# Performance work log

Measured on AMD Instinct MI355X. Metric: run time of the kernel, lower is better.

Reference implementation:

```python
import jax, jax.numpy as jnp
import numpy as np

C = 128
GROUPS = 8
EPS = 1e-5


def setup_inputs() -> dict:
    key = jax.random.key(0)
    ks = jax.random.split(key, 7)
    B, D, H, W = 2, 8, 32, 32
    x = jax.random.normal(ks[0], (B, C, D, H, W), dtype=jnp.float32)
    gamma = jnp.ones((C,), dtype=jnp.float32)
    beta = jnp.zeros((C,), dtype=jnp.float32)
    w_qkv = jax.random.normal(ks[1], (3 * C, C), dtype=jnp.float32) * 0.02
    b_qkv = jnp.zeros((3 * C,), dtype=jnp.float32)
    w_proj = jax.random.normal(ks[2], (C, C), dtype=jnp.float32) * 0.02
    b_proj = jnp.zeros((C,), dtype=jnp.float32)
    return {"x": x, "gamma": gamma, "beta": beta, "w_qkv": w_qkv,
            "b_qkv": b_qkv, "w_proj": w_proj, "b_proj": b_proj}


def _group_norm(x, gamma, beta):
    B, Cc, D, H, W = x.shape
    xg = x.reshape(B, GROUPS, Cc // GROUPS, D, H, W)
    mean = jnp.mean(xg, axis=(2, 3, 4, 5), keepdims=True)
    var = jnp.var(xg, axis=(2, 3, 4, 5), keepdims=True)
    xn = (xg - mean) * jax.lax.rsqrt(var + EPS)
    xn = xn.reshape(B, Cc, D, H, W)
    return xn * gamma[None, :, None, None, None] + beta[None, :, None, None, None]


def reference(x, gamma, beta, w_qkv, b_qkv, w_proj, b_proj):
    B, Cc, D, H, W = x.shape
    N = D * H * W
    h = _group_norm(x, gamma, beta)
    # 1x1x1 conv == per-voxel matmul over channels
    qkv = jnp.einsum('bcdhw,oc->bodhw', h, w_qkv) + b_qkv[None, :, None, None, None]
    q, k, v = jnp.split(qkv, 3, axis=1)  # each [B, C, D, H, W]
    q = q.reshape(B, Cc, N).transpose(0, 2, 1)  # [B, N, C]
    k = k.reshape(B, Cc, N).transpose(0, 2, 1)
    v = v.reshape(B, Cc, N).transpose(0, 2, 1)
    scale = Cc ** (-0.5)
    attn = jax.nn.softmax(jnp.einsum('bnc,bmc->bnm', q, k) * scale, axis=-1)
    h = jnp.einsum('bnm,bmc->bnc', attn, v)  # [B, N, C]
    h = h.transpose(0, 2, 1).reshape(B, Cc, D, H, W)
    out = jnp.einsum('bcdhw,oc->bodhw', h, w_proj) + b_proj[None, :, None, None, None]
    return x + out
```

## Files before the change

### kernel.cpp

```cpp
#include <hip/hip_runtime.h>

typedef __bf16 bf16x8 __attribute__((ext_vector_type(8)));
typedef float  f32x4  __attribute__((ext_vector_type(4)));
typedef float  f32x16 __attribute__((ext_vector_type(16)));
typedef float  f32x2  __attribute__((ext_vector_type(2)));
typedef unsigned int uint32;
typedef unsigned int u32x2 __attribute__((ext_vector_type(2)));
typedef int i32x4 __attribute__((ext_vector_type(4)));
typedef int i32x8 __attribute__((ext_vector_type(8)));
typedef long long i64;
typedef long long i64x4v __attribute__((ext_vector_type(4)));

#define MFMA16(a, b, c) __builtin_amdgcn_mfma_f32_16x16x32_bf16((a), (b), (c), 0, 0, 0)
#define MFMA32F8(a, b, c) __builtin_amdgcn_mfma_f32_32x32x16_fp8_fp8((a), (b), (c), 0, 0, 0)
#define GLL(gsrc, ldst) __builtin_amdgcn_global_load_lds( \
    (const __attribute__((address_space(1))) uint32*)(gsrc), \
    (__attribute__((address_space(3))) uint32*)(ldst), 16, 0, 0)

static constexpr int Cch = 128;
static constexpr int Nvox = 8192;

__device__ inline f32x16 mx4(i32x8 a, i32x8 b, f32x16 c) {
#if __has_builtin(__builtin_amdgcn_mfma_scale_f32_32x32x64_f8f6f4)
  return __builtin_amdgcn_mfma_scale_f32_32x32x64_f8f6f4(
      a, b, c, 0 , 0 ,
      0, 0x7F7F7F7Fu ,
      0, 0x7F7F7F7Fu );
#else
  i64x4v av = __builtin_bit_cast(i64x4v, a);
  i64x4v bv = __builtin_bit_cast(i64x4v, b);
  c = MFMA32F8(av[0], bv[0], c);
  c = MFMA32F8(av[1], bv[1], c);
  c = MFMA32F8(av[2], bv[2], c);
  c = MFMA32F8(av[3], bv[3], c);
  return c;
#endif
}

__device__ inline unsigned int pkbf(float x, float y) {
  unsigned short ux = __builtin_bit_cast(unsigned short, (__bf16)x);
  unsigned short uy = __builtin_bit_cast(unsigned short, (__bf16)y);
  return (unsigned int)ux | ((unsigned int)uy << 16);
}

__device__ inline unsigned int pk4fp8(float a, float b, float c, float d) {
  int w = 0;
  w = __builtin_amdgcn_cvt_pk_fp8_f32(a, b, w, false);
  w = __builtin_amdgcn_cvt_pk_fp8_f32(c, d, w, true);
  return (unsigned int)w;
}
__device__ inline unsigned char fp8b(float x) {
  return (unsigned char)(__builtin_amdgcn_cvt_pk_fp8_f32(x, x, 0, false) & 0xff);
}

__device__ inline void lane32_swap(unsigned int& x, unsigned int& y) {
#if __has_builtin(__builtin_amdgcn_permlane32_swap)
  auto r = __builtin_amdgcn_permlane32_swap(x, y, false, false);
  x = r[0]; y = r[1];
#else
  unsigned int sx = (unsigned int)__shfl_xor((int)x, 32);
  unsigned int sy = (unsigned int)__shfl_xor((int)y, 32);
  bool lo = ((threadIdx.x & 63) < 32);
  unsigned int nx = lo ? x : sy;
  unsigned int ny = lo ? sx : y;
  x = nx; y = ny;
#endif
}
__device__ inline float red32_sum(float v) {
  unsigned int a = __builtin_bit_cast(unsigned int, v), b = a;
  lane32_swap(a, b);
  return __builtin_bit_cast(float, a) + __builtin_bit_cast(float, b);
}

__global__ __launch_bounds__(256) void gn_part_k(const float* __restrict__ x,
                                                 f32x2* __restrict__ part) {
  int bg = blockIdx.x >> 4, pt = blockIdx.x & 15;
  const f32x4* xb = (const f32x4*)(x + (size_t)bg * 131072 + (size_t)pt * 8192);
  float s = 0.f, ss = 0.f;
  for (int i = threadIdx.x; i < 2048; i += 256) {
    f32x4 v = xb[i];
    s += (v.x + v.y) + (v.z + v.w);
    ss += (v.x * v.x + v.y * v.y) + (v.z * v.z + v.w * v.w);
  }
#pragma unroll
  for (int off = 32; off; off >>= 1) {
    s  += __shfl_down(s, off);
    ss += __shfl_down(ss, off);
  }
  __shared__ float rb[4], rbss[4];
  if ((threadIdx.x & 63) == 0) { rb[threadIdx.x >> 6] = s; rbss[threadIdx.x >> 6] = ss; }
  __syncthreads();
  if (threadIdx.x == 0) {
    f32x2 o; o.x = rb[0] + rb[1] + rb[2] + rb[3];
    o.y = rbss[0] + rbss[1] + rbss[2] + rbss[3];
    part[blockIdx.x] = o;
  }
}

__global__ __launch_bounds__(256) void gn_fin_k(const f32x2* __restrict__ part,
                                                float* __restrict__ stats) {
  int tid = threadIdx.x;
  f32x2 v = part[tid];
  float s = v.x, ss = v.y;
#pragma unroll
  for (int off = 1; off < 16; off <<= 1) {
    s += __shfl_xor(s, off);
    ss += __shfl_xor(ss, off);
  }
  if ((tid & 15) == 0) {
    int bg = tid >> 4;
    const float invn = 1.f / 131072.f;
    float mean = s * invn;
    float var = ss * invn - mean * mean;
    stats[bg] = mean;
    stats[16 + bg] = rsqrtf(var + 1e-5f);
  }
}

__global__ __launch_bounds__(256) void conv_w_k(const float* __restrict__ wq,
                                                const float* __restrict__ wp,
                                                __bf16* __restrict__ wqb,
                                                __bf16* __restrict__ wpb) {
  int i = blockIdx.x * 256 + threadIdx.x;
  if (i < 384 * 128) wqb[i] = (__bf16)wq[i];
  if (i < 128 * 128) wpb[i] = (__bf16)wp[i];
}

__global__ __launch_bounds__(256) void gn_apply_k(const float* __restrict__ x,
                                                  const float* __restrict__ gamma,
                                                  const float* __restrict__ beta,
                                                  const float* __restrict__ stats,
                                                  __bf16* __restrict__ xn) {
  __shared__ __bf16 t[64][136];
  int b = blockIdx.x >> 7;
  int n0 = (blockIdx.x & 127) << 6;
  const float* xb = x + (size_t)b * Cch * Nvox;
  for (int i = threadIdx.x; i < 128 * 64; i += 256) {
    int c = i >> 6, nl = i & 63;
    int g = c >> 4;
    float mean = stats[b * 8 + g];
    float rstd = stats[16 + b * 8 + g];
    float v = xb[(size_t)c * Nvox + n0 + nl];
    t[nl][c] = (__bf16)((v - mean) * rstd * gamma[c] + beta[c]);
  }
  __syncthreads();
  __bf16* outb = xn + (size_t)b * Nvox * Cch;
  for (int i = threadIdx.x; i < 64 * 16; i += 256) {
    int row = i >> 4, ch = (i & 15) << 3;
    *reinterpret_cast<bf16x8*>(&outb[(size_t)(n0 + row) * Cch + ch]) =
        *reinterpret_cast<const bf16x8*>(&t[row][ch]);
  }
}

__global__ __launch_bounds__(256) void qkv_k(const __bf16* __restrict__ xn,
                                             const __bf16* __restrict__ wq,
                                             const float* __restrict__ b_qkv,
                                             unsigned char* __restrict__ q8,
                                             unsigned char* __restrict__ k8,
                                             unsigned char* __restrict__ v8t) {
  int id = blockIdx.x;
  int b = id / 768;
  int rr = id % 768;
  int o0b = (rr >> 7) * 64;
  int n0 = (rr & 127) * 64;
  int w = threadIdx.x >> 6, l = threadIdx.x & 63;
  int lr = l & 15, lh = l >> 4;
  int ow = o0b + w * 16;
  const float k2 = 0.08838834764831845f * 1.4426950408889634f;

  bf16x8 a[4];
#pragma unroll
  for (int kc = 0; kc < 4; kc++)
    a[kc] = *reinterpret_cast<const bf16x8*>(&wq[(size_t)(ow + lr) * 128 + kc * 32 + lh * 8]);

  const __bf16* xb = xn + (size_t)b * Nvox * Cch;
#pragma unroll
  for (int ns = 0; ns < 4; ns++) {
    f32x4 acc = {0.f, 0.f, 0.f, 0.f};
#pragma unroll
    for (int kc = 0; kc < 4; kc++) {
      bf16x8 bf = *reinterpret_cast<const bf16x8*>(
          &xb[(size_t)(n0 + ns * 16 + lr) * Cch + kc * 32 + lh * 8]);
      acc = MFMA16(a[kc], bf, acc);
    }
    int o0 = ow + lh * 4;
    int n = n0 + ns * 16 + lr;
    float f0 = acc[0] + b_qkv[o0 + 0];
    float f1 = acc[1] + b_qkv[o0 + 1];
    float f2 = acc[2] + b_qkv[o0 + 2];
    float f3 = acc[3] + b_qkv[o0 + 3];
    if (o0 < 128) {
      *reinterpret_cast<unsigned int*>(
          q8 + ((size_t)b * Nvox + n) * 128 + o0) =
          pk4fp8(f0 * k2, f1 * k2, f2 * k2, f3 * k2);
    } else if (o0 < 256) {
      *reinterpret_cast<unsigned int*>(
          k8 + ((size_t)b * Nvox + n) * 128 + (o0 - 128)) = pk4fp8(f0, f1, f2, f3);
    } else {
      int c0 = o0 - 256;
      int kk = n & 63;
      int r4 = kk & 15;
      int hh = (r4 >> 2) & 1;
      int jj = (r4 & 3) + (((r4 >> 3) & 1) << 2);
      int m = ((kk >> 5) << 5) + (hh << 4) + (((kk >> 4) & 1) << 3) + jj;
      int nst = (n & ~63) | m;
      v8t[((size_t)b * Cch + c0 + 0) * Nvox + nst] = fp8b(f0);
      v8t[((size_t)b * Cch + c0 + 1) * Nvox + nst] = fp8b(f1);
      v8t[((size_t)b * Cch + c0 + 2) * Nvox + nst] = fp8b(f2);
      v8t[((size_t)b * Cch + c0 + 3) * Nvox + nst] = fp8b(f3);
    }
  }
}

__global__ __launch_bounds__(256, 2) void attn_k(const unsigned char* __restrict__ q,
                                                 const unsigned char* __restrict__ kk,
                                                 const unsigned char* __restrict__ vt,
                                                 __bf16* __restrict__ po0,
                                                 __bf16* __restrict__ po1,
                                                 __bf16* __restrict__ po2,
                                                 __bf16* __restrict__ po3,
                                                 f32x2* __restrict__ ml) {
  extern __shared__ char smem[];
  const int bi = blockIdx.x;
  const int kq = bi & 3;
  const int b = (bi >> 2) & 1;
  const int qgrp = bi >> 3;
  const int w = threadIdx.x >> 6;
  const int l = threadIdx.x & 63;
  const int l31 = l & 31, h = l >> 5;
  const int swl16 = (l31 & 15) << 4;

  const char* kbase = (const char*)kk + ((size_t)b * 8192 + (size_t)kq * 2048) * 128;
  const char* vbase = (const char*)vt + (size_t)b * 1048576 + (size_t)kq * 2048;

  const unsigned char* qrow = q +
      ((size_t)b * 8192 + (size_t)qgrp * 128 + (size_t)w * 32 + l31) * 128 + h * 32;
  i32x8 qa8[2];
#pragma unroll
  for (int dc = 0; dc < 2; dc++) {
    i32x4 q0 = *reinterpret_cast<const i32x4*>(qrow + dc * 64);
    i32x4 q1 = *reinterpret_cast<const i32x4*>(qrow + dc * 64 + 16);
    qa8[dc] = __builtin_shufflevector(q0, q1, 0, 1, 2, 3, 4, 5, 6, 7);
  }

  f32x16 O[4];
#pragma unroll
  for (int cb = 0; cb < 4; cb++)
#pragma unroll
    for (int r = 0; r < 16; r++) O[cb][r] = 0.f;
  float s0 = 0.f, s1 = 0.f, s2 = 0.f, s3 = 0.f;

  auto stage = [&](int t, int bs) {
    if (w < 2) {
      const char* kt = kbase + (size_t)t * 64 * 128;
      char* dst = smem + bs * 16384;
#pragma unroll
      for (int it = 0; it < 4; ++it) {
        int ob = (w * 4 + it) * 1024;
        int o = ob + l * 16;
        int row = o >> 8;
        int lcol = (o & 255) ^ ((row & 15) << 4);
        int ksel = lcol >> 7, c = lcol & 127;
        GLL(kt + (size_t)(ksel * 32 + row) * 128 + c, dst + ob);
      }
    } else {
      const char* vtile = vbase + (size_t)t * 64;
      char* dst = smem + bs * 16384 + 8192;
#pragma unroll
      for (int it = 0; it < 4; ++it) {
        int ob = ((w - 2) * 4 + it) * 1024;
        int o = ob + l * 16;
        int row = o >> 8;
        int lcol = (o & 255) ^ ((row & 15) << 4);
        int cs = lcol >> 6, k16 = lcol & 63;
        GLL(vtile + (size_t)(cs * 32 + row) * 8192 + k16, dst + ob);
      }
    }
  };

  stage(0, 0);
  int cur = 0;
  const int NT = 32;

  for (int t = 0; t < NT; ++t) {
    asm volatile("s_waitcnt vmcnt(0) lgkmcnt(0)" ::: "memory");
    __builtin_amdgcn_sched_barrier(0);
    __syncthreads();
    if (t + 1 < NT) stage(t + 1, cur ^ 1);

    const char* Kb = smem + cur * 16384;
    const char* Vb = Kb + 8192;

    f32x16 St[2];
#pragma unroll
    for (int ks = 0; ks < 2; ks++)
#pragma unroll
      for (int r = 0; r < 16; r++) St[ks][r] = 0.f;
    __builtin_amdgcn_s_setprio(1);
#pragma unroll
    for (int ks = 0; ks < 2; ks++) {
#pragma unroll
      for (int dc = 0; dc < 2; dc++) {
        int base = ks * 128 + dc * 64 + h * 32;
        i32x4 k0 = *reinterpret_cast<const i32x4*>(
            Kb + (size_t)l31 * 256 + (base ^ swl16));
        i32x4 k1 = *reinterpret_cast<const i32x4*>(
            Kb + (size_t)l31 * 256 + ((base + 16) ^ swl16));
        St[ks] = mx4(__builtin_shufflevector(k0, k1, 0, 1, 2, 3, 4, 5, 6, 7),
                     qa8[dc], St[ks]);
      }
    }
    __builtin_amdgcn_s_setprio(0);

#pragma unroll
    for (int ks = 0; ks < 2; ks++)
#pragma unroll
      for (int r = 0; r < 16; r++)
        St[ks][r] = __builtin_amdgcn_exp2f(St[ks][r]);
#pragma unroll
    for (int ks = 0; ks < 2; ks++)
#pragma unroll
      for (int r = 0; r < 16; r += 4) {
        s0 += St[ks][r + 0]; s1 += St[ks][r + 1];
        s2 += St[ks][r + 2]; s3 += St[ks][r + 3];
      }

    i32x8 pb;
#pragma unroll
    for (int ks = 0; ks < 2; ks++) {
      pb[ks * 4 + 0] = (int)pk4fp8(St[ks][0],  St[ks][1],  St[ks][2],  St[ks][3]);
      pb[ks * 4 + 1] = (int)pk4fp8(St[ks][4],  St[ks][5],  St[ks][6],  St[ks][7]);
      pb[ks * 4 + 2] = (int)pk4fp8(St[ks][8],  St[ks][9],  St[ks][10], St[ks][11]);
      pb[ks * 4 + 3] = (int)pk4fp8(St[ks][12], St[ks][13], St[ks][14], St[ks][15]);
    }

    __builtin_amdgcn_s_setprio(1);
#pragma unroll
    for (int cb = 0; cb < 4; cb++) {
      int vb0 = cb * 64 + h * 16;
      i32x4 v0 = *reinterpret_cast<const i32x4*>(
          Vb + (size_t)l31 * 256 + (vb0 ^ swl16));
      i32x4 v1 = *reinterpret_cast<const i32x4*>(
          Vb + (size_t)l31 * 256 + ((vb0 + 32) ^ swl16));
      O[cb] = mx4(__builtin_shufflevector(v0, v1, 0, 1, 2, 3, 4, 5, 6, 7),
                  pb, O[cb]);
    }
    __builtin_amdgcn_s_setprio(0);
    cur ^= 1;
  }

  float lsum = red32_sum((s0 + s1) + (s2 + s3));
  __bf16* po = (kq == 0) ? po0 : (kq == 1) ? po1 : (kq == 2) ? po2 : po3;
  int qg = b * 8192 + qgrp * 128 + w * 32 + l31;
#pragma unroll
  for (int cb = 0; cb < 4; cb++) {
#pragma unroll
    for (int rq = 0; rq < 4; rq++) {
      int c = cb * 32 + rq * 8 + h * 4;
      u32x2 wv;
      wv[0] = pkbf(O[cb][rq * 4 + 0], O[cb][rq * 4 + 1]);
      wv[1] = pkbf(O[cb][rq * 4 + 2], O[cb][rq * 4 + 3]);
      *reinterpret_cast<u32x2*>((char*)po + ((size_t)qg * 128 + c) * 2) = wv;
    }
  }
  if (l < 32) {
    f32x2 v; v.x = 0.f; v.y = lsum;
    ml[(size_t)kq * 16384 + qg] = v;
  }
}

__global__ __launch_bounds__(256) void proj_k(const __bf16* __restrict__ po0,
                                              const __bf16* __restrict__ po1,
                                              const __bf16* __restrict__ po2,
                                              const __bf16* __restrict__ po3,
                                              const f32x2* __restrict__ ml,
                                              const __bf16* __restrict__ wp,
                                              const float* __restrict__ b_proj,
                                              const float* __restrict__ x,
                                              float* __restrict__ out) {
  int id = blockIdx.x;
  int b = id >> 8;
  int co0 = ((id >> 7) & 1) * 64;
  int n0 = (id & 127) * 64;
  int w = threadIdx.x >> 6, l = threadIdx.x & 63;
  int lr = l & 15, lh = l >> 4;
  int cow = co0 + w * 16;

  bf16x8 a[4];
#pragma unroll
  for (int kc = 0; kc < 4; kc++)
    a[kc] = *reinterpret_cast<const bf16x8*>(&wp[(size_t)(cow + lr) * 128 + kc * 32 + lh * 8]);

#pragma unroll
  for (int ns = 0; ns < 4; ns++) {
    int n = n0 + ns * 16 + lr;
    int qg = b * 8192 + n;
    f32x2 a0 = ml[qg], a1 = ml[16384 + qg], a2 = ml[32768 + qg], a3 = ml[49152 + qg];
    float M = fmaxf(fmaxf(a0.x, a1.x), fmaxf(a2.x, a3.x));
    float e0 = __builtin_amdgcn_exp2f(a0.x - M);
    float e1 = __builtin_amdgcn_exp2f(a1.x - M);
    float e2 = __builtin_amdgcn_exp2f(a2.x - M);
    float e3 = __builtin_amdgcn_exp2f(a3.x - M);
    float invL = 1.f / (e0 * a0.y + e1 * a1.y + e2 * a2.y + e3 * a3.y);
    float c0f = e0 * invL, c1f = e1 * invL, c2f = e2 * invL, c3f = e3 * invL;

    f32x4 acc = {0.f, 0.f, 0.f, 0.f};
#pragma unroll
    for (int kc = 0; kc < 4; kc++) {
      size_t off = (size_t)qg * 128 + kc * 32 + lh * 8;
      bf16x8 v0 = *reinterpret_cast<const bf16x8*>(&po0[off]);
      bf16x8 v1 = *reinterpret_cast<const bf16x8*>(&po1[off]);
      bf16x8 v2 = *reinterpret_cast<const bf16x8*>(&po2[off]);
      bf16x8 v3 = *reinterpret_cast<const bf16x8*>(&po3[off]);
      bf16x8 hv;
#pragma unroll
      for (int i = 0; i < 8; i++)
        hv[i] = (__bf16)(c0f * (float)v0[i] + c1f * (float)v1[i] +
                         c2f * (float)v2[i] + c3f * (float)v3[i]);
      acc = MFMA16(a[kc], hv, acc);
    }
#pragma unroll
    for (int r2 = 0; r2 < 4; r2++) {
      int co = cow + lh * 4 + r2;
      size_t idx = ((size_t)b * Cch + co) * Nvox + n;
      out[idx] = x[idx] + b_proj[co] + acc[r2];
    }
  }
}

extern "C" void kernel_launch(void* const* d_in, const int* in_sizes, int n_in,
                              void* d_out, int out_size, void* d_ws, size_t ws_size,
                              hipStream_t stream) {
  const float* x      = (const float*)d_in[0];
  const float* gamma  = (const float*)d_in[1];
  const float* beta   = (const float*)d_in[2];
  const float* w_qkv  = (const float*)d_in[3];
  const float* b_qkv  = (const float*)d_in[4];
  const float* w_proj = (const float*)d_in[5];
  const float* b_proj = (const float*)d_in[6];
  float* out = (float*)d_out;

  char* ws = (char*)d_ws;
  float*  stats = (float*)ws;
  f32x2*  part  = (f32x2*)(ws + 256);
  __bf16* wq_b  = (__bf16*)(ws + 4096);
  __bf16* wp_b  = (__bf16*)(ws + 4096 + 98304);
  size_t base = 135168;
  const size_t SZ = (size_t)2 * Nvox * Cch * sizeof(__bf16);
  __bf16* xn  = (__bf16*)(ws + base + 0 * SZ);
  unsigned char* q8  = (unsigned char*)(ws + base + 1 * SZ);
  unsigned char* k8  = (unsigned char*)(ws + base + 2 * SZ);
  unsigned char* v8t = (unsigned char*)(ws + base + 3 * SZ);
  __bf16* hw  = (__bf16*)(ws + base + 4 * SZ);
  f32x2*  ml  = (f32x2*)(ws + base + 5 * SZ);
  __bf16* po2 = (__bf16*)(ws + base + 5 * SZ + 524288);
  __bf16* po3 = (__bf16*)(ws + base + 5 * SZ + 524288 + SZ);

  (void)hipFuncSetAttribute((const void*)attn_k,
                            hipFuncAttributeMaxDynamicSharedMemorySize, 32768);

  gn_part_k<<<256, 256, 0, stream>>>(x, part);
  gn_fin_k<<<1, 256, 0, stream>>>(part, stats);
  conv_w_k<<<192, 256, 0, stream>>>(w_qkv, w_proj, wq_b, wp_b);
  gn_apply_k<<<256, 256, 0, stream>>>(x, gamma, beta, stats, xn);
  qkv_k<<<1536, 256, 0, stream>>>(xn, wq_b, b_qkv, q8, k8, v8t);
  attn_k<<<512, 256, 32768, stream>>>(q8, k8, v8t, hw, xn, po2, po3, ml);
  proj_k<<<512, 256, 0, stream>>>(hw, xn, po2, po3, ml, wp_b, b_proj, x, out);
}
```

Before: 96.83 us.

## Split attention KV into eight chunks, store fp8 partials, fuse small prep kernels

Attention now splits keys into 8 chunks of 1024 instead of 4 of 2048, launches 1024 blocks with a launch bound of 4 blocks per unit, and writes partial outputs as fp8 plus a single row-sum float. The max term was already fixed at zero, so the proj kernel just sums the partials and divides by the total L. The weight conversion kernel is folded into gn_part_k, and the group-norm finalize kernel is folded into gn_apply_k, removing two launches. The goal is better occupancy and less partial-output traffic, at the cost of fp8 rounding on the partial outputs and redundant stats work in every apply block.

```diff
diff --git a/kernel.cpp b/kernel.cpp
--- a/kernel.cpp
+++ b/kernel.cpp
@@ -24,8 +24,7 @@
 #if __has_builtin(__builtin_amdgcn_mfma_scale_f32_32x32x64_f8f6f4)
   return __builtin_amdgcn_mfma_scale_f32_32x32x64_f8f6f4(
       a, b, c, 0 , 0 ,
-      0, 0x7F7F7F7Fu ,
-      0, 0x7F7F7F7Fu );
+      0, 0x7F7F7F7Fu, 0, 0x7F7F7F7Fu );
 #else
   i64x4v av = __builtin_bit_cast(i64x4v, a);
   i64x4v bv = __builtin_bit_cast(i64x4v, b);
@@ -37,12 +36,6 @@
 #endif
 }
 
-__device__ inline unsigned int pkbf(float x, float y) {
-  unsigned short ux = __builtin_bit_cast(unsigned short, (__bf16)x);
-  unsigned short uy = __builtin_bit_cast(unsigned short, (__bf16)y);
-  return (unsigned int)ux | ((unsigned int)uy << 16);
-}
-
 __device__ inline unsigned int pk4fp8(float a, float b, float c, float d) {
   int w = 0;
   w = __builtin_amdgcn_cvt_pk_fp8_f32(a, b, w, false);
@@ -51,6 +44,22 @@
 }
 __device__ inline unsigned char fp8b(float x) {
   return (unsigned char)(__builtin_amdgcn_cvt_pk_fp8_f32(x, x, 0, false) & 0xff);
+}
+template <bool HI>
+__device__ inline f32x2 dec2fp8(unsigned int w) {
+#if __has_builtin(__builtin_amdgcn_cvt_pk_f32_fp8)
+  return __builtin_amdgcn_cvt_pk_f32_fp8((int)w, HI);
+#else
+  f32x2 r;
+#pragma unroll
+  for (int j = 0; j < 2; j++) {
+    unsigned char v = (unsigned char)(w >> ((HI ? 2 : 0) + j) * 8);
+    unsigned int e = (v >> 3) & 15, m = v & 7;
+    float mag = e ? ldexpf((float)(8 + m), (int)e - 10) : ldexpf((float)m, -9);
+    r[j] = (v & 0x80) ? -mag : mag;
+  }
+  return r;
+#endif
 }
 
 __device__ inline void lane32_swap(unsigned int& x, unsigned int& y) {
@@ -73,7 +82,15 @@
 }
 
 __global__ __launch_bounds__(256) void gn_part_k(const float* __restrict__ x,
-                                                 f32x2* __restrict__ part) {
+                                                 f32x2* __restrict__ part,
+                                                 const float* __restrict__ wq,
+                                                 const float* __restrict__ wp,
+                                                 __bf16* __restrict__ wqb,
+                                                 __bf16* __restrict__ wpb) {
+  int wi = blockIdx.x * 256 + threadIdx.x;
+  if (wi < 49152) wqb[wi] = (__bf16)wq[wi];
+  else wpb[wi - 49152] = (__bf16)wp[wi - 49152];
+
   int bg = blockIdx.x >> 4, pt = blockIdx.x & 15;
   const f32x4* xb = (const f32x4*)(x + (size_t)bg * 131072 + (size_t)pt * 8192);
   float s = 0.f, ss = 0.f;
@@ -97,49 +114,40 @@
   }
 }
 
-__global__ __launch_bounds__(256) void gn_fin_k(const f32x2* __restrict__ part,
-                                                float* __restrict__ stats) {
-  int tid = threadIdx.x;
-  f32x2 v = part[tid];
-  float s = v.x, ss = v.y;
-#pragma unroll
-  for (int off = 1; off < 16; off <<= 1) {
-    s += __shfl_xor(s, off);
-    ss += __shfl_xor(ss, off);
-  }
-  if ((tid & 15) == 0) {
-    int bg = tid >> 4;
-    const float invn = 1.f / 131072.f;
-    float mean = s * invn;
-    float var = ss * invn - mean * mean;
-    stats[bg] = mean;
-    stats[16 + bg] = rsqrtf(var + 1e-5f);
-  }
-}
-
-__global__ __launch_bounds__(256) void conv_w_k(const float* __restrict__ wq,
-                                                const float* __restrict__ wp,
-                                                __bf16* __restrict__ wqb,
-                                                __bf16* __restrict__ wpb) {
-  int i = blockIdx.x * 256 + threadIdx.x;
-  if (i < 384 * 128) wqb[i] = (__bf16)wq[i];
-  if (i < 128 * 128) wpb[i] = (__bf16)wp[i];
-}
-
 __global__ __launch_bounds__(256) void gn_apply_k(const float* __restrict__ x,
                                                   const float* __restrict__ gamma,
                                                   const float* __restrict__ beta,
-                                                  const float* __restrict__ stats,
+                                                  const f32x2* __restrict__ part,
                                                   __bf16* __restrict__ xn) {
   __shared__ __bf16 t[64][136];
+  __shared__ float sm_mean[16], sm_rstd[16];
+  int tid = threadIdx.x;
+  {
+    f32x2 v = part[tid];
+    float s = v.x, ss = v.y;
+#pragma unroll
+    for (int off = 1; off < 16; off <<= 1) {
+      s += __shfl_xor(s, off);
+      ss += __shfl_xor(ss, off);
+    }
+    if ((tid & 15) == 0) {
+      int bg = tid >> 4;
+      const float invn = 1.f / 131072.f;
+      float mean = s * invn;
+      float var = ss * invn - mean * mean;
+      sm_mean[bg] = mean;
+      sm_rstd[bg] = rsqrtf(var + 1e-5f);
+    }
+  }
+  __syncthreads();
   int b = blockIdx.x >> 7;
   int n0 = (blockIdx.x & 127) << 6;
   const float* xb = x + (size_t)b * Cch * Nvox;
   for (int i = threadIdx.x; i < 128 * 64; i += 256) {
     int c = i >> 6, nl = i & 63;
     int g = c >> 4;
-    float mean = stats[b * 8 + g];
-    float rstd = stats[16 + b * 8 + g];
+    float mean = sm_mean[b * 8 + g];
+    float rstd = sm_rstd[b * 8 + g];
     float v = xb[(size_t)c * Nvox + n0 + nl];
     t[nl][c] = (__bf16)((v - mean) * rstd * gamma[c] + beta[c]);
   }
@@ -212,26 +220,23 @@
   }
 }
 
-__global__ __launch_bounds__(256, 2) void attn_k(const unsigned char* __restrict__ q,
+__global__ __launch_bounds__(256, 4) void attn_k(const unsigned char* __restrict__ q,
                                                  const unsigned char* __restrict__ kk,
                                                  const unsigned char* __restrict__ vt,
-                                                 __bf16* __restrict__ po0,
-                                                 __bf16* __restrict__ po1,
-                                                 __bf16* __restrict__ po2,
-                                                 __bf16* __restrict__ po3,
-                                                 f32x2* __restrict__ ml) {
+                                                 unsigned char* __restrict__ po8,
+                                                 float* __restrict__ mlf) {
   extern __shared__ char smem[];
   const int bi = blockIdx.x;
-  const int kq = bi & 3;
-  const int b = (bi >> 2) & 1;
-  const int qgrp = bi >> 3;
+  const int kq = bi & 7;
+  const int b = (bi >> 3) & 1;
+  const int qgrp = bi >> 4;
   const int w = threadIdx.x >> 6;
   const int l = threadIdx.x & 63;
   const int l31 = l & 31, h = l >> 5;
   const int swl16 = (l31 & 15) << 4;
 
-  const char* kbase = (const char*)kk + ((size_t)b * 8192 + (size_t)kq * 2048) * 128;
-  const char* vbase = (const char*)vt + (size_t)b * 1048576 + (size_t)kq * 2048;
+  const char* kbase = (const char*)kk + ((size_t)b * 8192 + (size_t)kq * 1024) * 128;
+  const char* vbase = (const char*)vt + (size_t)b * 1048576 + (size_t)kq * 1024;
 
   const unsigned char* qrow = q +
       ((size_t)b * 8192 + (size_t)qgrp * 128 + (size_t)w * 32 + l31) * 128 + h * 32;
@@ -280,7 +285,7 @@
 
   stage(0, 0);
   int cur = 0;
-  const int NT = 32;
+  const int NT = 16;
 
   for (int t = 0; t < NT; ++t) {
     asm volatile("s_waitcnt vmcnt(0) lgkmcnt(0)" ::: "memory");
@@ -350,30 +355,23 @@
   }
 
   float lsum = red32_sum((s0 + s1) + (s2 + s3));
-  __bf16* po = (kq == 0) ? po0 : (kq == 1) ? po1 : (kq == 2) ? po2 : po3;
+  unsigned char* po = po8 + (size_t)kq * 2097152;
   int qg = b * 8192 + qgrp * 128 + w * 32 + l31;
 #pragma unroll
   for (int cb = 0; cb < 4; cb++) {
 #pragma unroll
     for (int rq = 0; rq < 4; rq++) {
       int c = cb * 32 + rq * 8 + h * 4;
-      u32x2 wv;
-      wv[0] = pkbf(O[cb][rq * 4 + 0], O[cb][rq * 4 + 1]);
-      wv[1] = pkbf(O[cb][rq * 4 + 2], O[cb][rq * 4 + 3]);
-      *reinterpret_cast<u32x2*>((char*)po + ((size_t)qg * 128 + c) * 2) = wv;
-    }
-  }
-  if (l < 32) {
-    f32x2 v; v.x = 0.f; v.y = lsum;
-    ml[(size_t)kq * 16384 + qg] = v;
-  }
-}
-
-__global__ __launch_bounds__(256) void proj_k(const __bf16* __restrict__ po0,
-                                              const __bf16* __restrict__ po1,
-                                              const __bf16* __restrict__ po2,
-                                              const __bf16* __restrict__ po3,
-                                              const f32x2* __restrict__ ml,
+      *reinterpret_cast<unsigned int*>(po + (size_t)qg * 128 + c) =
+          pk4fp8(O[cb][rq * 4 + 0], O[cb][rq * 4 + 1],
+                 O[cb][rq * 4 + 2], O[cb][rq * 4 + 3]);
+    }
+  }
+  if (l < 32) mlf[(size_t)kq * 16384 + qg] = lsum;
+}
+
+__global__ __launch_bounds__(256) void proj_k(const unsigned char* __restrict__ po8,
+                                              const float* __restrict__ mlf,
                                               const __bf16* __restrict__ wp,
                                               const float* __restrict__ b_proj,
                                               const float* __restrict__ x,
@@ -395,28 +393,33 @@
   for (int ns = 0; ns < 4; ns++) {
     int n = n0 + ns * 16 + lr;
     int qg = b * 8192 + n;
-    f32x2 a0 = ml[qg], a1 = ml[16384 + qg], a2 = ml[32768 + qg], a3 = ml[49152 + qg];
-    float M = fmaxf(fmaxf(a0.x, a1.x), fmaxf(a2.x, a3.x));
-    float e0 = __builtin_amdgcn_exp2f(a0.x - M);
-    float e1 = __builtin_amdgcn_exp2f(a1.x - M);
-    float e2 = __builtin_amdgcn_exp2f(a2.x - M);
-    float e3 = __builtin_amdgcn_exp2f(a3.x - M);
-    float invL = 1.f / (e0 * a0.y + e1 * a1.y + e2 * a2.y + e3 * a3.y);
-    float c0f = e0 * invL, c1f = e1 * invL, c2f = e2 * invL, c3f = e3 * invL;
+    float L = 0.f;
+#pragma unroll
+    for (int i = 0; i < 8; i++) L += mlf[(size_t)i * 16384 + qg];
+    float invL = 1.f / L;
 
     f32x4 acc = {0.f, 0.f, 0.f, 0.f};
 #pragma unroll
     for (int kc = 0; kc < 4; kc++) {
-      size_t off = (size_t)qg * 128 + kc * 32 + lh * 8;
-      bf16x8 v0 = *reinterpret_cast<const bf16x8*>(&po0[off]);
-      bf16x8 v1 = *reinterpret_cast<const bf16x8*>(&po1[off]);
-      bf16x8 v2 = *reinterpret_cast<const bf16x8*>(&po2[off]);
-      bf16x8 v3 = *reinterpret_cast<const bf16x8*>(&po3[off]);
+      float hv8[8];
+#pragma unroll
+      for (int j = 0; j < 8; j++) hv8[j] = 0.f;
+#pragma unroll
+      for (int i = 0; i < 8; i++) {
+        u32x2 wv = *reinterpret_cast<const u32x2*>(
+            po8 + (size_t)i * 2097152 + (size_t)qg * 128 + kc * 32 + lh * 8);
+        f32x2 p0 = dec2fp8<false>(wv[0]);
+        f32x2 p1 = dec2fp8<true>(wv[0]);
+        f32x2 p2 = dec2fp8<false>(wv[1]);
+        f32x2 p3 = dec2fp8<true>(wv[1]);
+        hv8[0] += p0[0]; hv8[1] += p0[1];
+        hv8[2] += p1[0]; hv8[3] += p1[1];
+        hv8[4] += p2[0]; hv8[5] += p2[1];
+        hv8[6] += p3[0]; hv8[7] += p3[1];
+      }
       bf16x8 hv;
 #pragma unroll
-      for (int i = 0; i < 8; i++)
-        hv[i] = (__bf16)(c0f * (float)v0[i] + c1f * (float)v1[i] +
-                         c2f * (float)v2[i] + c3f * (float)v3[i]);
+      for (int j = 0; j < 8; j++) hv[j] = (__bf16)(hv8[j] * invL);
       acc = MFMA16(a[kc], hv, acc);
     }
 #pragma unroll
@@ -441,7 +444,6 @@
   float* out = (float*)d_out;
 
   char* ws = (char*)d_ws;
-  float*  stats = (float*)ws;
   f32x2*  part  = (f32x2*)(ws + 256);
   __bf16* wq_b  = (__bf16*)(ws + 4096);
   __bf16* wp_b  = (__bf16*)(ws + 4096 + 98304);
@@ -451,19 +453,15 @@
   unsigned char* q8  = (unsigned char*)(ws + base + 1 * SZ);
   unsigned char* k8  = (unsigned char*)(ws + base + 2 * SZ);
   unsigned char* v8t = (unsigned char*)(ws + base + 3 * SZ);
-  __bf16* hw  = (__bf16*)(ws + base + 4 * SZ);
-  f32x2*  ml  = (f32x2*)(ws + base + 5 * SZ);
-  __bf16* po2 = (__bf16*)(ws + base + 5 * SZ + 524288);
-  __bf16* po3 = (__bf16*)(ws + base + 5 * SZ + 524288 + SZ);
+  unsigned char* po8 = (unsigned char*)(ws + base + 4 * SZ);
+  float* mlf = (float*)(ws + base + 8 * SZ);
 
   (void)hipFuncSetAttribute((const void*)attn_k,
                             hipFuncAttributeMaxDynamicSharedMemorySize, 32768);
 
-  gn_part_k<<<256, 256, 0, stream>>>(x, part);
-  gn_fin_k<<<1, 256, 0, stream>>>(part, stats);
-  conv_w_k<<<192, 256, 0, stream>>>(w_qkv, w_proj, wq_b, wp_b);
-  gn_apply_k<<<256, 256, 0, stream>>>(x, gamma, beta, stats, xn);
+  gn_part_k<<<256, 256, 0, stream>>>(x, part, w_qkv, w_proj, wq_b, wp_b);
+  gn_apply_k<<<256, 256, 0, stream>>>(x, gamma, beta, part, xn);
   qkv_k<<<1536, 256, 0, stream>>>(xn, wq_b, b_qkv, q8, k8, v8t);
-  attn_k<<<512, 256, 32768, stream>>>(q8, k8, v8t, hw, xn, po2, po3, ml);
-  proj_k<<<512, 256, 0, stream>>>(hw, xn, po2, po3, ml, wp_b, b_proj, x, out);
-}
+  attn_k<<<1024, 256, 32768, stream>>>(q8, k8, v8t, po8, mlf);
+  proj_k<<<512, 256, 0, stream>>>(po8, mlf, wp_b, b_proj, x, out);
+}
```

Result: slower. 311.8 us (+222.0%).
